# Performance work log

Measured on AMD Instinct MI355X. Metric: run time of the kernel, lower is better.

## Reference

```python
import jax, jax.numpy as jnp
import numpy as np

B, S, E, H = 4, 1024, 1024, 16
D = E // H  # head dim = 64

def setup_inputs() -> dict:
    key = jax.random.key(0)
    k1, k2, k3, k4, k5 = jax.random.split(key, 5)
    return {
        "lstm_out": jax.random.normal(k1, (B, S, E), dtype=jnp.float32),
        "in_proj_weight": jax.random.normal(k2, (3 * E, E), dtype=jnp.float32) * 0.02,
        "in_proj_bias": jax.random.normal(k3, (3 * E,), dtype=jnp.float32) * 0.02,
        "out_proj_weight": jax.random.normal(k4, (E, E), dtype=jnp.float32) * 0.02,
        "out_proj_bias": jax.random.normal(k5, (E,), dtype=jnp.float32) * 0.02,
    }

def reference(lstm_out, in_proj_weight, in_proj_bias, out_proj_weight, out_proj_bias):
    # Packed QKV projection, as in nn.MultiheadAttention (Linear uses x @ W.T + b)
    qkv = lstm_out @ in_proj_weight.T + in_proj_bias          # [B,S,3E]
    q, k, v = jnp.split(qkv, 3, axis=-1)                      # each [B,S,E]
    def heads(t):
        return t.reshape(B, S, H, D).transpose(0, 2, 1, 3)    # [B,H,S,D]
    q, k, v = heads(q), heads(k), heads(v)
    scale = 1.0 / jnp.sqrt(jnp.asarray(D, dtype=q.dtype))
    scores = jnp.einsum("bhsd,bhtd->bhst", q * scale, k)      # [B,H,S,S]
    attn = jax.nn.softmax(scores, axis=-1)                    # [B,H,S,S]
    ctx = jnp.einsum("bhst,bhtd->bhsd", attn, v)              # [B,H,S,D]
    ctx = ctx.transpose(0, 2, 1, 3).reshape(B, S, E)          # [B,S,E]
    attn_output = ctx @ out_proj_weight.T + out_proj_bias     # [B,S,E]
    # need_weights=True with default average_attn_weights=True -> mean over heads
    attn_weights = attn.mean(axis=1)                          # [B,S,S]
    context_vector = attn_output.mean(axis=1)                 # [B,E]
    return (context_vector, attn_weights)
```

## Files before the change

### kernel.cpp

```cpp
#include <hip/hip_runtime.h>


typedef unsigned short u16;
using s16x8 = __attribute__((ext_vector_type(8))) short;
using f32x4 = __attribute__((ext_vector_type(4))) float;
using u16x4 = __attribute__((ext_vector_type(4))) unsigned short;

#define AS1 __attribute__((address_space(1)))
#define AS3 __attribute__((address_space(3)))

#define QSCALE 0.1803368801111204f

__device__ __forceinline__ u16 f2bf(float f) {
    unsigned u = __float_as_uint(f);
    u += 0x7fffu + ((u >> 16) & 1u);
    return (u16)(u >> 16);
}

__global__ void k_prep(const float* __restrict__ X, const float* __restrict__ W1,
                       u16* __restrict__ Xb, u16* __restrict__ W1b,
                       float* __restrict__ cmean) {
    int i = blockIdx.x * blockDim.x + threadIdx.x;
    const float* src; u16* dst; int off;
    if (i < 1048576)       { src = X;  dst = Xb;  off = i; }
    else                   { src = W1; dst = W1b; off = i - 1048576; }
    float4 v = reinterpret_cast<const float4*>(src)[off];
    u16x4 o = { f2bf(v.x), f2bf(v.y), f2bf(v.z), f2bf(v.w) };
    reinterpret_cast<u16x4*>(dst)[off] = o;
    if (i < 4096) cmean[i] = 0.f;
}

__global__ __launch_bounds__(512) void k_gemm_bt(
    const u16* __restrict__ A, const u16* __restrict__ B,
    const float* __restrict__ bias, u16* __restrict__ C,
    u16* __restrict__ vt) {
    const int K = 1024;
    const int nbx = gridDim.x;
    const int nwg = nbx * gridDim.y;
    const int bid = blockIdx.y * nbx + blockIdx.x;
    const int per = nwg >> 3;
    const int swz = (bid & 7) * per + (bid >> 3);
    const int n0 = (swz % nbx) * 128, m0 = (swz / nbx) * 128;
    const int tid = threadIdx.x, lane = tid & 63, w = tid >> 6;
    const int wm = w >> 1, wn = w & 1;
    const int g = lane >> 4, l15 = lane & 15;
    __shared__ __attribute__((aligned(16))) u16 As[2][128 * 64];
    __shared__ __attribute__((aligned(16))) u16 Bs[2][128 * 64];

    f32x4 acc[2][4];
    #pragma unroll
    for (int mi = 0; mi < 2; ++mi)
        #pragma unroll
        for (int nj = 0; nj < 4; ++nj) acc[mi][nj] = (f32x4){0.f, 0.f, 0.f, 0.f};

    auto STAGE = [&](int k0, int sb) {
        #pragma unroll
        for (int r = 0; r < 2; ++r) {
            int c = tid + r * 512;
            int row = c >> 3, j = c & 7;
            int js = j ^ (row & 7);
            __builtin_amdgcn_global_load_lds(
                (AS1 const void*)(A + (size_t)(m0 + row) * K + k0 + js * 8),
                (AS3 void*)(&As[sb][c * 8]), 16, 0, 0);
            __builtin_amdgcn_global_load_lds(
                (AS1 const void*)(B + (size_t)(n0 + row) * K + k0 + js * 8),
                (AS3 void*)(&Bs[sb][c * 8]), 16, 0, 0);
        }
    };

    STAGE(0, 0);
    int buf = 0;
    for (int k0 = 0; k0 < K; k0 += 64) {
        __syncthreads();
        if (k0 + 64 < K) STAGE(k0 + 64, buf ^ 1);
        #pragma unroll
        for (int kk = 0; kk < 64; kk += 32) {
            const int cx0 = (((kk >> 3) + g) ^ (l15 & 7)) * 8;
            s16x8 av[2], bv[4];
            #pragma unroll
            for (int mi = 0; mi < 2; ++mi)
                av[mi] = *reinterpret_cast<const s16x8*>(
                    &As[buf][(wm * 32 + mi * 16 + l15) * 64 + cx0]);
            #pragma unroll
            for (int nj = 0; nj < 4; ++nj)
                bv[nj] = *reinterpret_cast<const s16x8*>(
                    &Bs[buf][(wn * 64 + nj * 16 + l15) * 64 + cx0]);
            #pragma unroll
            for (int mi = 0; mi < 2; ++mi)
                #pragma unroll
                for (int nj = 0; nj < 4; ++nj)
                    acc[mi][nj] = __builtin_amdgcn_mfma_f32_16x16x32_bf16(av[mi], bv[nj], acc[mi][nj], 0, 0, 0);
        }
        buf ^= 1;
    }

    #pragma unroll
    for (int nj = 0; nj < 4; ++nj) {
        int n = n0 + wn * 64 + nj * 16 + l15;
        float scale = (n < 1024) ? QSCALE : 1.0f;
        float bvs = bias[n] * scale;
        if (n < 2048) {
            #pragma unroll
            for (int mi = 0; mi < 2; ++mi)
                #pragma unroll
                for (int i = 0; i < 4; ++i) {
                    int m = m0 + wm * 32 + mi * 16 + g * 4 + i;
                    C[(size_t)m * 2048 + n] = f2bf(acc[mi][nj][i] * scale + bvs);
                }
        } else {
            int hd = n - 2048;
            #pragma unroll
            for (int mi = 0; mi < 2; ++mi)
                #pragma unroll
                for (int i = 0; i < 4; ++i) {
                    int m = m0 + wm * 32 + mi * 16 + g * 4 + i;
                    int b = m >> 10, t = m & 1023;
                    vt[((size_t)(b * 16 + (hd >> 6)) * 64 + (hd & 63)) * 1024 + t] =
                        f2bf(acc[mi][nj][i] + bvs);
                }
        }
    }
}

__global__ __launch_bounds__(512, 2) void k_flash(const u16* __restrict__ qk,
                                                  const u16* __restrict__ vt,
                                                  float* __restrict__ ml,
                                                  float* __restrict__ cmean) {
    const int id = blockIdx.x + 8 * (blockIdx.y + 16 * blockIdx.z);
    const int x = id & 7, k = id >> 3;
    const int gbh = x * 8 + (k >> 3);
    const int qt = k & 7;
    const int b = gbh >> 4, h = gbh & 15;
    const int q0 = qt * 128;
    const int tid = threadIdx.x, lane = tid & 63, w = tid >> 6;
    const int g = lane >> 4, l15 = lane & 15;
    __shared__ __attribute__((aligned(16))) u16 Ks[2][64 * 64];
    __shared__ __attribute__((aligned(16))) u16 Vt[2][64 * 64];
    __shared__ __attribute__((aligned(16))) u16 Ps[8][16 * 64];

    const size_t rowQ = (size_t)(b * 1024 + q0 + w * 16 + l15) * 2048 + h * 64;
    const s16x8 qa0 = *reinterpret_cast<const s16x8*>(qk + rowQ + g * 8);
    const s16x8 qa1 = *reinterpret_cast<const s16x8*>(qk + rowQ + 32 + g * 8);
    const s16x8 onesv = { (short)0x3F80, (short)0x3F80, (short)0x3F80, (short)0x3F80,
                          (short)0x3F80, (short)0x3F80, (short)0x3F80, (short)0x3F80 };

    const int rowA = tid >> 3, jA = tid & 7;
    const int dKA = tid * 8;
    const u16* kbase0 = qk + (size_t)(b * 1024) * 2048 + 1024 + h * 64;
    const u16* vtb = vt + (size_t)(b * 16 + h) * 65536;
    const u16* gKA = kbase0 + (size_t)rowA * 2048 + ((jA ^ (rowA & 7)) * 8);
    const u16* gVA = vtb + (size_t)rowA * 1024 + ((jA ^ (rowA & 7)) * 8);

    int kO[2][4], vO[2], pO[2], pW[4];
    #pragma unroll
    for (int tj = 0; tj < 4; ++tj) {
        int trow = tj * 16 + l15;
        kO[0][tj] = trow * 64 + ((g ^ (trow & 7)) * 8);
        kO[1][tj] = trow * 64 + (((4 + g) ^ (trow & 7)) * 8);
        pW[tj] = l15 * 64 + (((tj * 2 + (g >> 1)) ^ (l15 & 7)) * 8) + (g & 1) * 4;
    }
    pO[0] = l15 * 64 + ((g ^ (l15 & 7)) * 8);
    pO[1] = l15 * 64 + (((4 + g) ^ (l15 & 7)) * 8);
    vO[0] = pO[0];
    vO[1] = pO[1];

    __builtin_amdgcn_global_load_lds((AS1 const void*)gKA, (AS3 void*)(&Ks[0][dKA]), 16, 0, 0);
    __builtin_amdgcn_global_load_lds((AS1 const void*)gVA, (AS3 void*)(&Vt[0][dKA]), 16, 0, 0);
    gKA += 64 * 2048; gVA += 64;

    f32x4 ctxa[4];
    #pragma unroll
    for (int nj = 0; nj < 4; ++nj) ctxa[nj] = (f32x4){0.f, 0.f, 0.f, 0.f};
    f32x4 lacc = (f32x4){0.f, 0.f, 0.f, 0.f};

    int buf = 0;
    for (int kt = 0; kt < 16; ++kt) {
        __syncthreads();
        if (kt < 15) {
            __builtin_amdgcn_global_load_lds((AS1 const void*)gKA, (AS3 void*)(&Ks[buf ^ 1][dKA]), 16, 0, 0);
            __builtin_amdgcn_global_load_lds((AS1 const void*)gVA, (AS3 void*)(&Vt[buf ^ 1][dKA]), 16, 0, 0);
            gKA += 64 * 2048; gVA += 64;
        }
        const u16* Kb = &Ks[buf][0];
        const u16* Vb = &Vt[buf][0];
        u16* Pw = &Ps[w][0];

        f32x4 sc[4];
        #pragma unroll
        for (int tj = 0; tj < 4; ++tj) sc[tj] = (f32x4){0.f, 0.f, 0.f, 0.f};
        __builtin_amdgcn_s_setprio(1);
        #pragma unroll
        for (int kki = 0; kki < 2; ++kki) {
            s16x8 qa = kki ? qa1 : qa0;
            #pragma unroll
            for (int tj = 0; tj < 4; ++tj) {
                s16x8 kb = *reinterpret_cast<const s16x8*>(Kb + kO[kki][tj]);
                sc[tj] = __builtin_amdgcn_mfma_f32_16x16x32_bf16(kb, qa, sc[tj], 0, 0, 0);
            }
        }
        __builtin_amdgcn_s_setprio(0);

        #pragma unroll
        for (int tj = 0; tj < 4; ++tj)
            #pragma unroll
            for (int i = 0; i < 4; ++i)
                sc[tj][i] = exp2f(sc[tj][i]);

        #pragma unroll
        for (int tj = 0; tj < 4; ++tj) {
            unsigned pk01, pk23;
            asm("v_cvt_pk_bf16_f32 %0, %1, %2" : "=v"(pk01) : "v"(sc[tj][0]), "v"(sc[tj][1]));
            asm("v_cvt_pk_bf16_f32 %0, %1, %2" : "=v"(pk23) : "v"(sc[tj][2]), "v"(sc[tj][3]));
            uint2 pk = { pk01, pk23 };
            *reinterpret_cast<uint2*>(Pw + pW[tj]) = pk;
        }

        __builtin_amdgcn_s_setprio(1);
        #pragma unroll
        for (int kki = 0; kki < 2; ++kki) {
            s16x8 pa = *reinterpret_cast<const s16x8*>(Pw + pO[kki]);
            lacc = __builtin_amdgcn_mfma_f32_16x16x32_bf16(pa, onesv, lacc, 0, 0, 0);
            #pragma unroll
            for (int nj = 0; nj < 4; ++nj) {
                s16x8 vb = *reinterpret_cast<const s16x8*>(Vb + nj * 1024 + vO[kki]);
                ctxa[nj] = __builtin_amdgcn_mfma_f32_16x16x32_bf16(pa, vb, ctxa[nj], 0, 0, 0);
            }
        }
        __builtin_amdgcn_s_setprio(0);
        buf ^= 1;
    }

    float inv_i[4];
    #pragma unroll
    for (int i = 0; i < 4; ++i) {
        inv_i[i] = 1.0f / lacc[i];
        if (l15 == 0)
            ml[(size_t)(b * 16 + h) * 1024 + q0 + w * 16 + g * 4 + i] = inv_i[i] * 0.0625f;
    }

    #pragma unroll
    for (int nj = 0; nj < 4; ++nj) {
        float s = ctxa[nj][0] * inv_i[0] + ctxa[nj][1] * inv_i[1]
                + ctxa[nj][2] * inv_i[2] + ctxa[nj][3] * inv_i[3];
        s += __shfl_xor(s, 16);
        s += __shfl_xor(s, 32);
        if (g == 0)
            atomicAdd(&cmean[b * 1024 + h * 64 + nj * 16 + l15], s * (1.0f / 1024.0f));
    }
}

__global__ __launch_bounds__(256, 4) void k_attnw(const u16* __restrict__ qk,
                                                  const float* __restrict__ ml,
                                                  float* __restrict__ attnw) {
    const int tt = blockIdx.x, stp = blockIdx.y, b = blockIdx.z;
    const int s0a = stp * 128, t0 = tt * 64;
    const int tid = threadIdx.x, lane = tid & 63, w = tid >> 6;
    const int g = lane >> 4, l15 = lane & 15;
    __shared__ __attribute__((aligned(16))) u16 Ks[2][64 * 64];
    __shared__ float mls[16][128];

    #pragma unroll
    for (int r = 0; r < 8; ++r) {
        int idx = tid + r * 256;
        int hh = idx >> 7, row = idx & 127;
        mls[hh][row] = ml[(size_t)(b * 16 + hh) * 1024 + s0a + row];
    }

    const int cA = tid, cB = tid + 256;
    const int rowA = cA >> 3, jA = cA & 7, rowB = cB >> 3, jB = cB & 7;
    const u16* kbase = qk + (size_t)(b * 1024 + t0) * 2048 + 1024;
    const size_t rowQa = (size_t)(b * 1024 + s0a + w * 16 + l15) * 2048;
    const size_t rowQb = rowQa + (size_t)64 * 2048;

    __builtin_amdgcn_global_load_lds((AS1 const void*)(kbase + (size_t)rowA * 2048 + ((jA ^ (rowA & 7)) * 8)),
                                     (AS3 void*)(&Ks[0][cA * 8]), 16, 0, 0);
    __builtin_amdgcn_global_load_lds((AS1 const void*)(kbase + (size_t)rowB * 2048 + ((jB ^ (rowB & 7)) * 8)),
                                     (AS3 void*)(&Ks[0][cB * 8]), 16, 0, 0);
    s16x8 qcA0 = *reinterpret_cast<const s16x8*>(qk + rowQa + g * 8);
    s16x8 qcA1 = *reinterpret_cast<const s16x8*>(qk + rowQa + 32 + g * 8);
    s16x8 qcB0 = *reinterpret_cast<const s16x8*>(qk + rowQb + g * 8);
    s16x8 qcB1 = *reinterpret_cast<const s16x8*>(qk + rowQb + 32 + g * 8);

    f32x4 accA[4], accB[4];
    #pragma unroll
    for (int tj = 0; tj < 4; ++tj) {
        accA[tj] = (f32x4){0.f, 0.f, 0.f, 0.f};
        accB[tj] = (f32x4){0.f, 0.f, 0.f, 0.f};
    }

    int buf = 0;
    for (int h = 0; h < 16; ++h) {
        __syncthreads();
        s16x8 qnA0, qnA1, qnB0, qnB1;
        if (h < 15) {
            const u16* kb2 = kbase + (h + 1) * 64;
            __builtin_amdgcn_global_load_lds((AS1 const void*)(kb2 + (size_t)rowA * 2048 + ((jA ^ (rowA & 7)) * 8)),
                                             (AS3 void*)(&Ks[buf ^ 1][cA * 8]), 16, 0, 0);
            __builtin_amdgcn_global_load_lds((AS1 const void*)(kb2 + (size_t)rowB * 2048 + ((jB ^ (rowB & 7)) * 8)),
                                             (AS3 void*)(&Ks[buf ^ 1][cB * 8]), 16, 0, 0);
            qnA0 = *reinterpret_cast<const s16x8*>(qk + rowQa + (h + 1) * 64 + g * 8);
            qnA1 = *reinterpret_cast<const s16x8*>(qk + rowQa + (h + 1) * 64 + 32 + g * 8);
            qnB0 = *reinterpret_cast<const s16x8*>(qk + rowQb + (h + 1) * 64 + g * 8);
            qnB1 = *reinterpret_cast<const s16x8*>(qk + rowQb + (h + 1) * 64 + 32 + g * 8);
        }

        f32x4 scA[4], scB[4];
        #pragma unroll
        for (int tj = 0; tj < 4; ++tj) {
            scA[tj] = (f32x4){0.f, 0.f, 0.f, 0.f};
            scB[tj] = (f32x4){0.f, 0.f, 0.f, 0.f};
        }
        #pragma unroll
        for (int kk = 0; kk < 64; kk += 32) {
            s16x8 qaA = kk ? qcA1 : qcA0;
            s16x8 qaB = kk ? qcB1 : qcB0;
            #pragma unroll
            for (int tj = 0; tj < 4; ++tj) {
                int trow = tj * 16 + l15;
                s16x8 kb = *reinterpret_cast<const s16x8*>(
                    &Ks[buf][trow * 64 + ((((kk >> 3) + g) ^ (trow & 7)) * 8)]);
                scA[tj] = __builtin_amdgcn_mfma_f32_16x16x32_bf16(qaA, kb, scA[tj], 0, 0, 0);
                scB[tj] = __builtin_amdgcn_mfma_f32_16x16x32_bf16(qaB, kb, scB[tj], 0, 0, 0);
            }
        }
        #pragma unroll
        for (int i = 0; i < 4; ++i) {
            int row = w * 16 + g * 4 + i;
            float Ma = mls[h][row];
            float Mb = mls[h][64 + row];
            #pragma unroll
            for (int tj = 0; tj < 4; ++tj) {
                accA[tj][i] += exp2f(scA[tj][i]) * Ma;
                accB[tj][i] += exp2f(scB[tj][i]) * Mb;
            }
        }
        qcA0 = qnA0; qcA1 = qnA1; qcB0 = qnB0; qcB1 = qnB1;
        buf ^= 1;
    }

    #pragma unroll
    for (int i = 0; i < 4; ++i) {
        int rowa = s0a + w * 16 + g * 4 + i;
        #pragma unroll
        for (int tj = 0; tj < 4; ++tj) {
            attnw[(size_t)(b * 1024 + rowa) * 1024 + t0 + tj * 16 + l15] = accA[tj][i];
            attnw[(size_t)(b * 1024 + rowa + 64) * 1024 + t0 + tj * 16 + l15] = accB[tj][i];
        }
    }
}

__global__ __launch_bounds__(256) void k_outproj(const float* __restrict__ cmean,
                                                 const float* __restrict__ wout,
                                                 const float* __restrict__ bias,
                                                 float* __restrict__ out) {
    __shared__ float cs[4096];
    #pragma unroll
    for (int r = 0; r < 16; ++r) {
        int idx = threadIdx.x + r * 256;
        cs[idx] = cmean[idx];
    }
    __syncthreads();
    int G = blockIdx.x * 256 + threadIdx.x;
    int e = G >> 4, ks = G & 15;
    const float4* wr = reinterpret_cast<const float4*>(wout) + (size_t)e * 256 + ks * 16;
    const float4* c0 = reinterpret_cast<const float4*>(&cs[0]) + ks * 16;
    const float4* c1 = reinterpret_cast<const float4*>(&cs[1024]) + ks * 16;
    const float4* c2 = reinterpret_cast<const float4*>(&cs[2048]) + ks * 16;
    const float4* c3 = reinterpret_cast<const float4*>(&cs[3072]) + ks * 16;
    float s0 = 0.f, s1 = 0.f, s2 = 0.f, s3 = 0.f;
    #pragma unroll
    for (int k = 0; k < 16; ++k) {
        float4 wv = wr[k];
        float4 a = c0[k], b = c1[k], c = c2[k], d = c3[k];
        s0 += a.x * wv.x + a.y * wv.y + a.z * wv.z + a.w * wv.w;
        s1 += b.x * wv.x + b.y * wv.y + b.z * wv.z + b.w * wv.w;
        s2 += c.x * wv.x + c.y * wv.y + c.z * wv.z + c.w * wv.w;
        s3 += d.x * wv.x + d.y * wv.y + d.z * wv.z + d.w * wv.w;
    }
    #pragma unroll
    for (int off = 1; off < 16; off <<= 1) {
        s0 += __shfl_xor(s0, off);
        s1 += __shfl_xor(s1, off);
        s2 += __shfl_xor(s2, off);
        s3 += __shfl_xor(s3, off);
    }
    if (ks == 0) {
        float bv = bias[e];
        out[e]        = s0 + bv;
        out[1024 + e] = s1 + bv;
        out[2048 + e] = s2 + bv;
        out[3072 + e] = s3 + bv;
    }
}

extern "C" void kernel_launch(void* const* d_in, const int* in_sizes, int n_in,
                              void* d_out, int out_size, void* d_ws, size_t ws_size,
                              hipStream_t stream) {
    const float* lstm = (const float*)d_in[0];
    const float* wqkv = (const float*)d_in[1];
    const float* bqkv = (const float*)d_in[2];
    const float* wout = (const float*)d_in[3];
    const float* bout = (const float*)d_in[4];
    float* out = (float*)d_out;

    char* ws = (char*)d_ws;
    u16*   Xbf   = (u16*)(ws);
    u16*   Wqkvb = (u16*)(ws + 8u  * 1024 * 1024);
    u16*   qkbuf = (u16*)(ws + 16u * 1024 * 1024);
    u16*   vtg   = (u16*)(ws + 32u * 1024 * 1024);
    float* ml    = (float*)(ws + 40u * 1024 * 1024);
    float* cmean = (float*)(ws + 41u * 1024 * 1024);

    k_prep<<<7168, 256, 0, stream>>>(lstm, wqkv, Xbf, Wqkvb, cmean);

    k_gemm_bt<<<dim3(24, 32), 512, 0, stream>>>(Xbf, Wqkvb, bqkv, qkbuf, vtg);
    k_flash<<<dim3(8, 16, 4), 512, 0, stream>>>(qkbuf, vtg, ml, cmean);
    k_attnw<<<dim3(16, 8, 4), 256, 0, stream>>>(qkbuf, ml, out + 4096);
    k_outproj<<<64, 256, 0, stream>>>(cmean, wout, bout, out);
}
```

Baseline: 120.4 us.

## Software-pipeline flash loop QK with previous tile's softmax-PV; widen outproj grid

The flash attention loop now computes QK^T scores for tile kt while doing exp/PV for tile kt-1, with a triple-buffered V tile in LDS so the V buffer stays valid across the extra iteration. The aim is to overlap MFMA score computation with the exp and P-store latency and give the scheduler independent work. Separately, the output-projection kernel uses 64 lanes per output row across 256 blocks instead of 16 lanes across 64 blocks, which spreads the weight reads over more blocks. The pipelining raises register pressure (a second set of score accumulators) and LDS use, which could hurt occupancy at 2 blocks per CU.

```diff
diff --git a/kernel.cpp b/kernel.cpp
--- a/kernel.cpp
+++ b/kernel.cpp
@@ -135,7 +135,7 @@
     const int tid = threadIdx.x, lane = tid & 63, w = tid >> 6;
     const int g = lane >> 4, l15 = lane & 15;
     __shared__ __attribute__((aligned(16))) u16 Ks[2][64 * 64];
-    __shared__ __attribute__((aligned(16))) u16 Vt[2][64 * 64];
+    __shared__ __attribute__((aligned(16))) u16 Vt[3][64 * 64];
     __shared__ __attribute__((aligned(16))) u16 Ps[8][16 * 64];
 
     const size_t rowQ = (size_t)(b * 1024 + q0 + w * 16 + l15) * 2048 + h * 64;
@@ -164,28 +164,12 @@
     vO[0] = pO[0];
     vO[1] = pO[1];
 
-    __builtin_amdgcn_global_load_lds((AS1 const void*)gKA, (AS3 void*)(&Ks[0][dKA]), 16, 0, 0);
-    __builtin_amdgcn_global_load_lds((AS1 const void*)gVA, (AS3 void*)(&Vt[0][dKA]), 16, 0, 0);
-    gKA += 64 * 2048; gVA += 64;
-
     f32x4 ctxa[4];
     #pragma unroll
     for (int nj = 0; nj < 4; ++nj) ctxa[nj] = (f32x4){0.f, 0.f, 0.f, 0.f};
     f32x4 lacc = (f32x4){0.f, 0.f, 0.f, 0.f};
 
-    int buf = 0;
-    for (int kt = 0; kt < 16; ++kt) {
-        __syncthreads();
-        if (kt < 15) {
-            __builtin_amdgcn_global_load_lds((AS1 const void*)gKA, (AS3 void*)(&Ks[buf ^ 1][dKA]), 16, 0, 0);
-            __builtin_amdgcn_global_load_lds((AS1 const void*)gVA, (AS3 void*)(&Vt[buf ^ 1][dKA]), 16, 0, 0);
-            gKA += 64 * 2048; gVA += 64;
-        }
-        const u16* Kb = &Ks[buf][0];
-        const u16* Vb = &Vt[buf][0];
-        u16* Pw = &Ps[w][0];
-
-        f32x4 sc[4];
+    auto QK = [&](const u16* Kb, f32x4* sc) {
         #pragma unroll
         for (int tj = 0; tj < 4; ++tj) sc[tj] = (f32x4){0.f, 0.f, 0.f, 0.f};
         __builtin_amdgcn_s_setprio(1);
@@ -199,13 +183,14 @@
             }
         }
         __builtin_amdgcn_s_setprio(0);
-
+    };
+    auto SMPV = [&](f32x4* sc, const u16* Vb) {
         #pragma unroll
         for (int tj = 0; tj < 4; ++tj)
             #pragma unroll
             for (int i = 0; i < 4; ++i)
                 sc[tj][i] = exp2f(sc[tj][i]);
-
+        u16* Pw = &Ps[w][0];
         #pragma unroll
         for (int tj = 0; tj < 4; ++tj) {
             unsigned pk01, pk23;
@@ -214,7 +199,6 @@
             uint2 pk = { pk01, pk23 };
             *reinterpret_cast<uint2*>(Pw + pW[tj]) = pk;
         }
-
         __builtin_amdgcn_s_setprio(1);
         #pragma unroll
         for (int kki = 0; kki < 2; ++kki) {
@@ -227,8 +211,36 @@
             }
         }
         __builtin_amdgcn_s_setprio(0);
-        buf ^= 1;
-    }
+    };
+
+    __builtin_amdgcn_global_load_lds((AS1 const void*)gKA, (AS3 void*)(&Ks[0][dKA]), 16, 0, 0);
+    __builtin_amdgcn_global_load_lds((AS1 const void*)gVA, (AS3 void*)(&Vt[0][dKA]), 16, 0, 0);
+    gKA += 64 * 2048; gVA += 64;
+
+    f32x4 scP[4];
+    __syncthreads();
+    __builtin_amdgcn_global_load_lds((AS1 const void*)gKA, (AS3 void*)(&Ks[1][dKA]), 16, 0, 0);
+    __builtin_amdgcn_global_load_lds((AS1 const void*)gVA, (AS3 void*)(&Vt[1][dKA]), 16, 0, 0);
+    gKA += 64 * 2048; gVA += 64;
+    QK(&Ks[0][0], scP);
+
+    #pragma unroll
+    for (int kt = 1; kt < 16; ++kt) {
+        __syncthreads();
+        if (kt < 15) {
+            __builtin_amdgcn_global_load_lds((AS1 const void*)gKA,
+                (AS3 void*)(&Ks[(kt + 1) & 1][dKA]), 16, 0, 0);
+            __builtin_amdgcn_global_load_lds((AS1 const void*)gVA,
+                (AS3 void*)(&Vt[(kt + 1) % 3][dKA]), 16, 0, 0);
+            gKA += 64 * 2048; gVA += 64;
+        }
+        f32x4 scC[4];
+        QK(&Ks[kt & 1][0], scC);
+        SMPV(scP, &Vt[(kt - 1) % 3][0]);
+        #pragma unroll
+        for (int tj = 0; tj < 4; ++tj) scP[tj] = scC[tj];
+    }
+    SMPV(scP, &Vt[15 % 3][0]);
 
     float inv_i[4];
     #pragma unroll
@@ -361,15 +373,15 @@
     }
     __syncthreads();
     int G = blockIdx.x * 256 + threadIdx.x;
-    int e = G >> 4, ks = G & 15;
-    const float4* wr = reinterpret_cast<const float4*>(wout) + (size_t)e * 256 + ks * 16;
-    const float4* c0 = reinterpret_cast<const float4*>(&cs[0]) + ks * 16;
-    const float4* c1 = reinterpret_cast<const float4*>(&cs[1024]) + ks * 16;
-    const float4* c2 = reinterpret_cast<const float4*>(&cs[2048]) + ks * 16;
-    const float4* c3 = reinterpret_cast<const float4*>(&cs[3072]) + ks * 16;
+    int e = G >> 6, ls = G & 63;
+    const float4* wr = reinterpret_cast<const float4*>(wout) + (size_t)e * 256 + ls * 4;
+    const float4* c0 = reinterpret_cast<const float4*>(&cs[0]) + ls * 4;
+    const float4* c1 = reinterpret_cast<const float4*>(&cs[1024]) + ls * 4;
+    const float4* c2 = reinterpret_cast<const float4*>(&cs[2048]) + ls * 4;
+    const float4* c3 = reinterpret_cast<const float4*>(&cs[3072]) + ls * 4;
     float s0 = 0.f, s1 = 0.f, s2 = 0.f, s3 = 0.f;
     #pragma unroll
-    for (int k = 0; k < 16; ++k) {
+    for (int k = 0; k < 4; ++k) {
         float4 wv = wr[k];
         float4 a = c0[k], b = c1[k], c = c2[k], d = c3[k];
         s0 += a.x * wv.x + a.y * wv.y + a.z * wv.z + a.w * wv.w;
@@ -378,13 +390,13 @@
         s3 += d.x * wv.x + d.y * wv.y + d.z * wv.z + d.w * wv.w;
     }
     #pragma unroll
-    for (int off = 1; off < 16; off <<= 1) {
+    for (int off = 1; off < 64; off <<= 1) {
         s0 += __shfl_xor(s0, off);
         s1 += __shfl_xor(s1, off);
         s2 += __shfl_xor(s2, off);
         s3 += __shfl_xor(s3, off);
     }
-    if (ks == 0) {
+    if (ls == 0) {
         float bv = bias[e];
         out[e]        = s0 + bv;
         out[1024 + e] = s1 + bv;
@@ -416,5 +428,5 @@
     k_gemm_bt<<<dim3(24, 32), 512, 0, stream>>>(Xbf, Wqkvb, bqkv, qkbuf, vtg);
     k_flash<<<dim3(8, 16, 4), 512, 0, stream>>>(qkbuf, vtg, ml, cmean);
     k_attnw<<<dim3(16, 8, 4), 256, 0, stream>>>(qkbuf, ml, out + 4096);
-    k_outproj<<<64, 256, 0, stream>>>(cmean, wout, bout, out);
-}
+    k_outproj<<<256, 256, 0, stream>>>(cmean, wout, bout, out);
+}
```

New measurement: 114.0 us (median of 3 runs). 5.3% less time.
